# Optimization experiments

Hardware: AMD Instinct MI355X
Metric: run time of the kernel (lower is better)

## Reference

```python
import jax, jax.numpy as jnp
import numpy as np

N, F, LEVELS, E = 100000, 128, 4, 500000


def setup_inputs() -> dict:
    key = jax.random.key(0)
    k1, k2, k3, k4, k5 = jax.random.split(key, 5)
    node_features = jax.random.normal(k1, (N, F), dtype=jnp.float32)
    W = jax.random.normal(k2, (LEVELS, F, F), dtype=jnp.float32) * 0.05  # nn.Linear weight [out,in] per level
    b = jax.random.normal(k3, (LEVELS, F), dtype=jnp.float32) * 0.02
    hierarchy_levels = jax.random.randint(k4, (N,), 0, 5, dtype=jnp.int32)
    hierarchy_edges = jax.random.randint(k5, (E, 2), 0, N, dtype=jnp.int32)
    return {"node_features": node_features, "W": W, "b": b,
            "hierarchy_levels": hierarchy_levels, "hierarchy_edges": hierarchy_edges}


def reference(node_features, W, b, hierarchy_levels, hierarchy_edges):
    levels = W.shape[0]
    lo = hierarchy_edges[:, 0]
    hi = hierarchy_edges[:, 1]
    ll = hierarchy_levels[lo]  # lower-node level per edge
    hl = hierarchy_levels[hi]  # higher-node level per edge
    valid = (ll >= 0) & (ll < levels) & (hl > ll)  # [E]
    x = node_features[lo]  # gather source features [E, F]
    # Group by level: one matmul per level over all edges, masked select (levels is small).
    prop = jnp.zeros_like(x)
    for l in range(levels):
        m = valid & (ll == l)
        yl = x @ W[l].T + b[l]  # Linear(feature_size, feature_size) at level l
        prop = prop + jnp.where(m[:, None], yl, jnp.zeros((), dtype=x.dtype))
    # scatter-add 0.2 * propagated into higher nodes
    agg = jax.ops.segment_sum(0.2 * prop, hi, num_segments=node_features.shape[0])
    return node_features + agg
```

## Files before the change

kernel.cpp:

```cpp
#include <hip/hip_runtime.h>
#include <hip/hip_bf16.h>

#define FDIM 128
#define NLEV 4
#define NT   64
#define WPAD 136

typedef unsigned int  u32;
typedef unsigned short u16;

typedef __attribute__((ext_vector_type(8))) short short8v;
typedef __attribute__((ext_vector_type(4))) float f32x4;

__device__ __forceinline__ float bf_lo(u32 p) { return __uint_as_float(p << 16); }
__device__ __forceinline__ float bf_hi(u32 p) { return __uint_as_float(p & 0xffff0000u); }
__device__ __forceinline__ u16 f2bf(float f) {
    u32 u = __float_as_uint(f);
    u32 r = (u + 0x7fffu + ((u >> 16) & 1u)) >> 16;
    return (u16)r;
}
__device__ __forceinline__ u32 pack2(float a, float b) {
    return (u32)f2bf(a) | ((u32)f2bf(b) << 16);
}

__global__ __launch_bounds__(256) void zero_kernel(int4* __restrict__ p, int n4) {
    int i = blockIdx.x * 256 + threadIdx.x;
    int stride = gridDim.x * 256;
    for (; i < n4; i += stride) p[i] = make_int4(0, 0, 0, 0);
}

__global__ __launch_bounds__(256) void binhist_kernel(
    const int* __restrict__ lv, int* __restrict__ cnt, int* __restrict__ bin,
    const int* __restrict__ edges, int* __restrict__ deg,
    int N, int E, int nodeBlocks)
{
    int t = threadIdx.x;
    int b = blockIdx.x;

    int e = b * 256 + t;
    if (e < E) {
        int lo = edges[2 * e];
        int hi = edges[2 * e + 1];
        if (lv[hi] > lv[lo]) atomicAdd(&deg[hi], 1);
    }

    if (b < nodeBlocks) {
        __shared__ int lcnt[NLEV];
        __shared__ int lbase[NLEV];
        if (t < NLEV) lcnt[t] = 0;
        __syncthreads();
        int n = b * 256 + t;
        int l = -1, pos = 0;
        if (n < N) {
            l = lv[n];
            if (l >= 0 && l < NLEV) pos = atomicAdd(&lcnt[l], 1);
            else l = -1;
        }
        __syncthreads();
        if (t < NLEV) lbase[t] = lcnt[t] ? atomicAdd(&cnt[t], lcnt[t]) : 0;
        __syncthreads();
        if (l >= 0) bin[l * N + lbase[l] + pos] = n;
    }
}

__global__ __launch_bounds__(256) void scan_local(const int* __restrict__ deg,
                                                  int* __restrict__ rowstart,
                                                  int* __restrict__ bsum, int N) {
    __shared__ int part[256];
    int t = threadIdx.x;
    int base = blockIdx.x * 1024 + t * 4;
    int v[4];
    #pragma unroll
    for (int k = 0; k < 4; ++k) v[k] = (base + k < N) ? deg[base + k] : 0;
    int s = v[0] + v[1] + v[2] + v[3];
    part[t] = s;
    __syncthreads();
    for (int off = 1; off < 256; off <<= 1) {
        int x = (t >= off) ? part[t - off] : 0;
        __syncthreads();
        part[t] += x;
        __syncthreads();
    }
    if (t == 255) bsum[blockIdx.x] = part[255];
    int run = part[t] - s;
    #pragma unroll
    for (int k = 0; k < 4; ++k) {
        if (base + k < N) rowstart[base + k] = run;
        run += v[k];
    }
}

__global__ __launch_bounds__(128) void scan_blocks(int* __restrict__ bsum, int nb) {
    __shared__ int s[128];
    int t = threadIdx.x;
    s[t] = (t < nb) ? bsum[t] : 0;
    __syncthreads();
    if (t == 0) {
        int run = 0;
        for (int i = 0; i < nb; ++i) { int v = s[i]; s[i] = run; run += v; }
    }
    __syncthreads();
    if (t < nb) bsum[t] = s[t];
}

__global__ __launch_bounds__(256) void fill_kernel(const int* __restrict__ edges,
                                                   const int* __restrict__ lv,
                                                   const int* __restrict__ rowstart,
                                                   const int* __restrict__ bsum,
                                                   int* __restrict__ ncur,
                                                   int* __restrict__ csr, int E) {
    int e = blockIdx.x * 256 + threadIdx.x;
    if (e >= E) return;
    int lo = edges[2 * e];
    int hi = edges[2 * e + 1];
    if (lv[hi] > lv[lo]) {
        int s = rowstart[hi] + bsum[hi >> 10] + atomicAdd(&ncur[hi], 1);
        csr[s] = lo;
    }
}

__global__ __launch_bounds__(256) void transform_kernel(
    const float* __restrict__ X, const float* __restrict__ Wg,
    const float* __restrict__ bg, const int* __restrict__ cnt,
    const int* __restrict__ bin, u16* __restrict__ Y, int N, int blocksPerLevel)
{
    __shared__ __align__(16) u16 Wt[FDIM][WPAD];
    __shared__ __align__(16) u16 Xt[NT][WPAD];
    __shared__ int nodes_s[NT];

    int l     = blockIdx.x / blocksPerLevel;
    int chunk = blockIdx.x % blocksPerLevel;
    int m_total = cnt[l];
    int base = chunk * NT;
    if (base >= m_total) return;
    int m = min(NT, m_total - base);
    int t = threadIdx.x;

    if (t < NT) nodes_s[t] = (t < m) ? bin[l * N + base + t] : -1;
    __syncthreads();

    const float4* Wl4 = (const float4*)(Wg + (size_t)l * FDIM * FDIM);
    #pragma unroll
    for (int k = 0; k < 16; ++k) {
        int flat4 = t + k * 256;
        int row = flat4 >> 5;
        int c4  = flat4 & 31;
        float4 v = Wl4[flat4];
        *(uint2*)&Wt[row][c4 * 4] = make_uint2(pack2(v.x, v.y), pack2(v.z, v.w));
    }
    #pragma unroll
    for (int k = 0; k < 8; ++k) {
        int flat4 = t + k * 256;
        int row = flat4 >> 5;
        int c4  = flat4 & 31;
        int node = nodes_s[row];
        float4 v = (node >= 0) ? ((const float4*)(X + (size_t)node * FDIM))[c4]
                               : make_float4(0.f, 0.f, 0.f, 0.f);
        *(uint2*)&Xt[row][c4 * 4] = make_uint2(pack2(v.x, v.y), pack2(v.z, v.w));
    }
    __syncthreads();

    int wid  = t >> 6;
    int lane = t & 63;
    int arow = lane & 15;
    int kgrp = lane >> 4;

    f32x4 acc[8];
    #pragma unroll
    for (int ft = 0; ft < 8; ++ft) acc[ft] = (f32x4){0.f, 0.f, 0.f, 0.f};

    #pragma unroll
    for (int kstep = 0; kstep < 4; ++kstep) {
        int k0 = kstep * 32 + kgrp * 8;
        short8v a = *(const short8v*)&Xt[wid * 16 + arow][k0];
        #pragma unroll
        for (int ft = 0; ft < 8; ++ft) {
            short8v b = *(const short8v*)&Wt[ft * 16 + arow][k0];
            acc[ft] = __builtin_amdgcn_mfma_f32_16x16x32_bf16(a, b, acc[ft], 0, 0, 0);
        }
    }

    const float* bl = bg + l * FDIM;
    #pragma unroll
    for (int ft = 0; ft < 8; ++ft) {
        float bv = bl[ft * 16 + arow];
        #pragma unroll
        for (int reg = 0; reg < 4; ++reg) {
            int r = wid * 16 + kgrp * 4 + reg;
            Xt[r][ft * 16 + arow] = f2bf(0.2f * (acc[ft][reg] + bv));
        }
    }
    __syncthreads();

    #pragma unroll
    for (int k = 0; k < 4; ++k) {
        int flat16 = t + k * 256;
        int row = flat16 >> 4;
        int c   = flat16 & 15;
        int node = nodes_s[row];
        if (node >= 0)
            *(uint4*)&Y[(size_t)node * FDIM + c * 8] = *(const uint4*)&Xt[row][c * 8];
    }
}

__global__ __launch_bounds__(256) void gather_kernel(
    const float* __restrict__ X, const uint2* __restrict__ Yp,
    const int* __restrict__ rowstart, const int* __restrict__ bsum,
    const int* __restrict__ deg, const int* __restrict__ csr,
    float* __restrict__ out, int N)
{
    int wid  = threadIdx.x >> 6;
    int lane = threadIdx.x & 63;
    int hl = lane >> 5;
    int sl = lane & 31;
    int node = blockIdx.x * 8 + wid * 2 + hl;
    if (node >= N) return;

    float4 xv = *(const float4*)&X[(size_t)node * FDIM + sl * 4];
    int row = rowstart[node] + bsum[node >> 10];
    int d   = deg[node];

    float a0 = 0.f, a1 = 0.f, a2 = 0.f, a3 = 0.f;
    for (int base = 0; base < d; base += 32) {
        int c = min(32, d - base);
        int myLo = (sl < c) ? csr[row + base + sl] : 0;
        for (int i = 0; i < c; i += 4) {
            int b = min(4, c - i);
            uint2 p[4];
            #pragma unroll
            for (int j = 0; j < 4; ++j) {
                if (j < b) {
                    int lo = __shfl(myLo, hl * 32 + i + j, 64);
                    p[j] = Yp[(size_t)lo * (FDIM / 4) + sl];
                }
            }
            #pragma unroll
            for (int j = 0; j < 4; ++j) {
                if (j < b) {
                    a0 += bf_lo(p[j].x); a1 += bf_hi(p[j].x);
                    a2 += bf_lo(p[j].y); a3 += bf_hi(p[j].y);
                }
            }
        }
    }
    float4 o = make_float4(xv.x + a0, xv.y + a1, xv.z + a2, xv.w + a3);
    *(float4*)&out[(size_t)node * FDIM + sl * 4] = o;
}

extern "C" void kernel_launch(void* const* d_in, const int* in_sizes, int n_in,
                              void* d_out, int out_size, void* d_ws, size_t ws_size,
                              hipStream_t stream) {
    const float* X  = (const float*)d_in[0];
    const float* Wg = (const float*)d_in[1];
    const float* bg = (const float*)d_in[2];
    const int*   lv = (const int*)d_in[3];
    const int*   eg = (const int*)d_in[4];
    float* out = (float*)d_out;

    int N = in_sizes[3];
    int E = in_sizes[4] / 2;

    char* p = (char*)d_ws;
    u16* Y        = (u16*)p;            p += (size_t)N * FDIM * sizeof(u16);
    int* cnt      = (int*)p;            p += 8 * sizeof(int);
    int* deg      = (int*)p;            p += (size_t)N * sizeof(int);
    int* ncur     = (int*)p;            p += (size_t)N * sizeof(int);
    int* rowstart = (int*)p;            p += (size_t)N * sizeof(int);
    int* bsum     = (int*)p;            p += 128 * sizeof(int);
    int* bin      = (int*)p;            p += (size_t)4 * N * sizeof(int);
    int* csr      = (int*)p;

    int nzero4 = (2 * N + 8) / 4;
    zero_kernel<<<196, 256, 0, stream>>>((int4*)cnt, nzero4);

    int nodeBlocks = (N + 255) / 256;
    int edgeBlocks = (E + 255) / 256;
    binhist_kernel<<<max(nodeBlocks, edgeBlocks), 256, 0, stream>>>(
        lv, cnt, bin, eg, deg, N, E, nodeBlocks);

    int nb = (N + 1023) / 1024;
    scan_local<<<nb, 256, 0, stream>>>(deg, rowstart, bsum, N);
    scan_blocks<<<1, 128, 0, stream>>>(bsum, nb);

    fill_kernel<<<edgeBlocks, 256, 0, stream>>>(eg, lv, rowstart, bsum, ncur, csr, E);

    int blocksPerLevel = (N + NT - 1) / NT;
    transform_kernel<<<NLEV * blocksPerLevel, 256, 0, stream>>>(
        X, Wg, bg, cnt, bin, Y, N, blocksPerLevel);

    gather_kernel<<<(N + 7) / 8, 256, 0, stream>>>(
        X, (const uint2*)Y, rowstart, bsum, deg, csr, out, N);
}
```

Before: 88.89 us.

## Fuse block-scan into scan_local and CSR fill into transform kernel

```diff
diff --git a/kernel.cpp b/kernel.cpp
--- a/kernel.cpp
+++ b/kernel.cpp
@@ -31,7 +31,7 @@
 
 __global__ __launch_bounds__(256) void binhist_kernel(
     const int* __restrict__ lv, int* __restrict__ cnt, int* __restrict__ bin,
-    const int* __restrict__ edges, int* __restrict__ deg,
+    const int2* __restrict__ edges2, int* __restrict__ deg,
     int N, int E, int nodeBlocks)
 {
     int t = threadIdx.x;
@@ -39,9 +39,8 @@
 
     int e = b * 256 + t;
     if (e < E) {
-        int lo = edges[2 * e];
-        int hi = edges[2 * e + 1];
-        if (lv[hi] > lv[lo]) atomicAdd(&deg[hi], 1);
+        int2 eg = edges2[e];
+        if (lv[eg.y] > lv[eg.x]) atomicAdd(&deg[eg.y], 1);
     }
 
     if (b < nodeBlocks) {
@@ -65,9 +64,12 @@
 
 __global__ __launch_bounds__(256) void scan_local(const int* __restrict__ deg,
                                                   int* __restrict__ rowstart,
-                                                  int* __restrict__ bsum, int N) {
+                                                  int* __restrict__ bsum,
+                                                  int* __restrict__ done, int N) {
     __shared__ int part[256];
+    __shared__ int iamlast;
     int t = threadIdx.x;
+    int nb = gridDim.x;
     int base = blockIdx.x * 1024 + t * 4;
     int v[4];
     #pragma unroll
@@ -88,56 +90,63 @@
         if (base + k < N) rowstart[base + k] = run;
         run += v[k];
     }
-}
-
-__global__ __launch_bounds__(128) void scan_blocks(int* __restrict__ bsum, int nb) {
-    __shared__ int s[128];
-    int t = threadIdx.x;
-    s[t] = (t < nb) ? bsum[t] : 0;
-    __syncthreads();
-    if (t == 0) {
-        int run = 0;
-        for (int i = 0; i < nb; ++i) { int v = s[i]; s[i] = run; run += v; }
-    }
-    __syncthreads();
-    if (t < nb) bsum[t] = s[t];
-}
-
-__global__ __launch_bounds__(256) void fill_kernel(const int* __restrict__ edges,
-                                                   const int* __restrict__ lv,
-                                                   const int* __restrict__ rowstart,
-                                                   const int* __restrict__ bsum,
-                                                   int* __restrict__ ncur,
-                                                   int* __restrict__ csr, int E) {
-    int e = blockIdx.x * 256 + threadIdx.x;
-    if (e >= E) return;
-    int lo = edges[2 * e];
-    int hi = edges[2 * e + 1];
-    if (lv[hi] > lv[lo]) {
-        int s = rowstart[hi] + bsum[hi >> 10] + atomicAdd(&ncur[hi], 1);
-        csr[s] = lo;
-    }
-}
-
-__global__ __launch_bounds__(256) void transform_kernel(
+
+    __threadfence();
+    __syncthreads();
+    if (t == 0) iamlast = (atomicAdd(done, 1) == nb - 1) ? 1 : 0;
+    __syncthreads();
+    if (iamlast) {
+        __threadfence();
+        int val = (t < nb) ? ((volatile int*)bsum)[t] : 0;
+        part[t] = val;
+        __syncthreads();
+        for (int off = 1; off < 256; off <<= 1) {
+            int x = (t >= off) ? part[t - off] : 0;
+            __syncthreads();
+            part[t] += x;
+            __syncthreads();
+        }
+        if (t < nb) bsum[t] = part[t] - val;
+    }
+}
+
+__global__ __launch_bounds__(256) void transform_fill_kernel(
     const float* __restrict__ X, const float* __restrict__ Wg,
     const float* __restrict__ bg, const int* __restrict__ cnt,
-    const int* __restrict__ bin, u16* __restrict__ Y, int N, int blocksPerLevel)
+    const int* __restrict__ bin, u16* __restrict__ Y,
+    const int2* __restrict__ edges2, const int* __restrict__ lv,
+    const int* __restrict__ rowstart, const int* __restrict__ bsum,
+    int* __restrict__ ncur, int* __restrict__ csr,
+    int N, int E, int blocksPerLevel, int transBlocks)
 {
+    int t = threadIdx.x;
+    int b = blockIdx.x;
+
+    if (b >= transBlocks) {
+        int e = (b - transBlocks) * 256 + t;
+        if (e < E) {
+            int2 eg = edges2[e];
+            int lo = eg.x, hi = eg.y;
+            if (lv[hi] > lv[lo]) {
+                int s = rowstart[hi] + bsum[hi >> 10] + atomicAdd(&ncur[hi], 1);
+                csr[s] = lo;
+            }
+        }
+        return;
+    }
+
     __shared__ __align__(16) u16 Wt[FDIM][WPAD];
-    __shared__ __align__(16) u16 Xt[NT][WPAD];
+    __shared__ __align__(16) u16 Ot[NT][WPAD];
     __shared__ int nodes_s[NT];
 
-    int l     = blockIdx.x / blocksPerLevel;
-    int chunk = blockIdx.x % blocksPerLevel;
+    int l     = b / blocksPerLevel;
+    int chunk = b % blocksPerLevel;
     int m_total = cnt[l];
     int base = chunk * NT;
     if (base >= m_total) return;
     int m = min(NT, m_total - base);
-    int t = threadIdx.x;
 
     if (t < NT) nodes_s[t] = (t < m) ? bin[l * N + base + t] : -1;
-    __syncthreads();
 
     const float4* Wl4 = (const float4*)(Wg + (size_t)l * FDIM * FDIM);
     #pragma unroll
@@ -148,16 +157,6 @@
         float4 v = Wl4[flat4];
         *(uint2*)&Wt[row][c4 * 4] = make_uint2(pack2(v.x, v.y), pack2(v.z, v.w));
     }
-    #pragma unroll
-    for (int k = 0; k < 8; ++k) {
-        int flat4 = t + k * 256;
-        int row = flat4 >> 5;
-        int c4  = flat4 & 31;
-        int node = nodes_s[row];
-        float4 v = (node >= 0) ? ((const float4*)(X + (size_t)node * FDIM))[c4]
-                               : make_float4(0.f, 0.f, 0.f, 0.f);
-        *(uint2*)&Xt[row][c4 * 4] = make_uint2(pack2(v.x, v.y), pack2(v.z, v.w));
-    }
     __syncthreads();
 
     int wid  = t >> 6;
@@ -165,6 +164,9 @@
     int arow = lane & 15;
     int kgrp = lane >> 4;
 
+    int node = nodes_s[wid * 16 + arow];
+    const float* xrow = X + (size_t)(node < 0 ? 0 : node) * FDIM;
+
     f32x4 acc[8];
     #pragma unroll
     for (int ft = 0; ft < 8; ++ft) acc[ft] = (f32x4){0.f, 0.f, 0.f, 0.f};
@@ -172,11 +174,19 @@
     #pragma unroll
     for (int kstep = 0; kstep < 4; ++kstep) {
         int k0 = kstep * 32 + kgrp * 8;
-        short8v a = *(const short8v*)&Xt[wid * 16 + arow][k0];
+        union { u32 u[4]; short8v v; } au;
+        if (node >= 0) {
+            float4 x0 = *(const float4*)&xrow[k0];
+            float4 x1 = *(const float4*)&xrow[k0 + 4];
+            au.u[0] = pack2(x0.x, x0.y); au.u[1] = pack2(x0.z, x0.w);
+            au.u[2] = pack2(x1.x, x1.y); au.u[3] = pack2(x1.z, x1.w);
+        } else {
+            au.u[0] = au.u[1] = au.u[2] = au.u[3] = 0;
+        }
         #pragma unroll
         for (int ft = 0; ft < 8; ++ft) {
-            short8v b = *(const short8v*)&Wt[ft * 16 + arow][k0];
-            acc[ft] = __builtin_amdgcn_mfma_f32_16x16x32_bf16(a, b, acc[ft], 0, 0, 0);
+            short8v bb = *(const short8v*)&Wt[ft * 16 + arow][k0];
+            acc[ft] = __builtin_amdgcn_mfma_f32_16x16x32_bf16(au.v, bb, acc[ft], 0, 0, 0);
         }
     }
 
@@ -187,7 +197,7 @@
         #pragma unroll
         for (int reg = 0; reg < 4; ++reg) {
             int r = wid * 16 + kgrp * 4 + reg;
-            Xt[r][ft * 16 + arow] = f2bf(0.2f * (acc[ft][reg] + bv));
+            Ot[r][ft * 16 + arow] = f2bf(0.2f * (acc[ft][reg] + bv));
         }
     }
     __syncthreads();
@@ -197,9 +207,9 @@
         int flat16 = t + k * 256;
         int row = flat16 >> 4;
         int c   = flat16 & 15;
-        int node = nodes_s[row];
-        if (node >= 0)
-            *(uint4*)&Y[(size_t)node * FDIM + c * 8] = *(const uint4*)&Xt[row][c * 8];
+        int nd = nodes_s[row];
+        if (nd >= 0)
+            *(uint4*)&Y[(size_t)nd * FDIM + c * 8] = *(const uint4*)&Ot[row][c * 8];
     }
 }
 
@@ -262,31 +272,31 @@
 
     char* p = (char*)d_ws;
     u16* Y        = (u16*)p;            p += (size_t)N * FDIM * sizeof(u16);
-    int* cnt      = (int*)p;            p += 8 * sizeof(int);
+    int* cnt      = (int*)p;            p += 16 * sizeof(int);
     int* deg      = (int*)p;            p += (size_t)N * sizeof(int);
     int* ncur     = (int*)p;            p += (size_t)N * sizeof(int);
     int* rowstart = (int*)p;            p += (size_t)N * sizeof(int);
     int* bsum     = (int*)p;            p += 128 * sizeof(int);
     int* bin      = (int*)p;            p += (size_t)4 * N * sizeof(int);
     int* csr      = (int*)p;
-
-    int nzero4 = (2 * N + 8) / 4;
-    zero_kernel<<<196, 256, 0, stream>>>((int4*)cnt, nzero4);
+    int* done     = cnt + 8;
+
+    int nzero4 = (2 * N + 16) / 4;
+    zero_kernel<<<(nzero4 + 255) / 256, 256, 0, stream>>>((int4*)cnt, nzero4);
 
     int nodeBlocks = (N + 255) / 256;
     int edgeBlocks = (E + 255) / 256;
     binhist_kernel<<<max(nodeBlocks, edgeBlocks), 256, 0, stream>>>(
-        lv, cnt, bin, eg, deg, N, E, nodeBlocks);
+        lv, cnt, bin, (const int2*)eg, deg, N, E, nodeBlocks);
 
     int nb = (N + 1023) / 1024;
-    scan_local<<<nb, 256, 0, stream>>>(deg, rowstart, bsum, N);
-    scan_blocks<<<1, 128, 0, stream>>>(bsum, nb);
-
-    fill_kernel<<<edgeBlocks, 256, 0, stream>>>(eg, lv, rowstart, bsum, ncur, csr, E);
+    scan_local<<<nb, 256, 0, stream>>>(deg, rowstart, bsum, done, N);
 
     int blocksPerLevel = (N + NT - 1) / NT;
-    transform_kernel<<<NLEV * blocksPerLevel, 256, 0, stream>>>(
-        X, Wg, bg, cnt, bin, Y, N, blocksPerLevel);
+    int transBlocks = NLEV * blocksPerLevel;
+    transform_fill_kernel<<<transBlocks + edgeBlocks, 256, 0, stream>>>(
+        X, Wg, bg, cnt, bin, Y, (const int2*)eg, lv, rowstart, bsum, ncur, csr,
+        N, E, blocksPerLevel, transBlocks);
 
     gather_kernel<<<(N + 7) / 8, 256, 0, stream>>>(
         X, (const uint2*)Y, rowstart, bsum, deg, csr, out, N);
```

Result: no change. 89.87 us (+1.1%).
